# Optimization experiments

Hardware: AMD Instinct MI355X
Metric: run time of the kernel (lower is better)

Reference implementation:

```python
import jax, jax.numpy as jnp
import numpy as np

D_MODEL = 1024
NUM_HEADS = 16
HEAD_DIM = D_MODEL // NUM_HEADS
BATCH = 2
SEQ = 2048


def setup_inputs() -> dict:
    key = jax.random.key(0)
    ks = jax.random.split(key, 9)
    s = 1.0 / np.sqrt(D_MODEL)
    inp = {
        "x": jax.random.normal(ks[0], (BATCH, SEQ, D_MODEL), dtype=jnp.float32),
        "mask": jnp.ones((BATCH, SEQ), dtype=jnp.int32),
        "Wq": jax.random.uniform(ks[1], (D_MODEL, D_MODEL), jnp.float32, -s, s),
        "bq": jax.random.uniform(ks[2], (D_MODEL,), jnp.float32, -s, s),
        "Wk": jax.random.uniform(ks[3], (D_MODEL, D_MODEL), jnp.float32, -s, s),
        "bk": jax.random.uniform(ks[4], (D_MODEL,), jnp.float32, -s, s),
        "Wv": jax.random.uniform(ks[5], (D_MODEL, D_MODEL), jnp.float32, -s, s),
        "bv": jax.random.uniform(ks[6], (D_MODEL,), jnp.float32, -s, s),
        "Wo": jax.random.uniform(ks[7], (D_MODEL, D_MODEL), jnp.float32, -s, s),
        "bo": jax.random.uniform(ks[8], (D_MODEL,), jnp.float32, -s, s),
    }
    return inp


def reference(x, mask, Wq, bq, Wk, bk, Wv, bv, Wo, bo):
    B, S, D = x.shape
    H, Hd = NUM_HEADS, HEAD_DIM
    # torch Linear: y = x @ W.T + b ; then reshape to [B, H, S, Hd]
    def proj(W, b):
        return (x @ W.T + b).reshape(B, S, H, Hd).transpose(0, 2, 1, 3)
    Q = proj(Wq, bq)
    K = proj(Wk, bk)
    V = proj(Wv, bv)
    scale = 1.0 / jnp.sqrt(jnp.asarray(Hd, dtype=x.dtype))
    scores = jnp.einsum("bhqd,bhkd->bhqk", Q, K) * scale  # [B,H,S,S]
    # mask [B,S] -> broadcast over query positions; masked_fill(mask==0, -1e9)
    scores = jnp.where(mask[:, None, None, :] == 0, jnp.asarray(-1e9, x.dtype), scores)
    attn = jax.nn.softmax(scores, axis=-1)
    context = jnp.einsum("bhqk,bhkd->bhqd", attn, V)
    context = context.transpose(0, 2, 1, 3).reshape(B, S, D)
    return context @ Wo.T + bo
```

## Files before the change

### kernel.cpp

```cpp
#include <hip/hip_runtime.h>
#include <hip/hip_bf16.h>
#include <cstdint>

#define D_MODEL 1024
#define NUM_HEADS 16
#define HEAD_DIM 64
#define BATCH 2
#define SEQ 2048
#define MROWS (BATCH * SEQ)

typedef __attribute__((ext_vector_type(8))) short bf16x8;
typedef __attribute__((ext_vector_type(4))) float f32x4;
typedef __attribute__((ext_vector_type(2))) unsigned u32x2;
typedef unsigned short u16;

#define QSCALE (0.125f * 1.44269504f)

#if __has_builtin(__builtin_amdgcn_exp2f)
#define EXP2F(x) __builtin_amdgcn_exp2f(x)
#else
#define EXP2F(x) exp2f(x)
#endif

static __device__ __forceinline__ u16 f2bf(float f) {
    unsigned int u = __float_as_uint(f);
    unsigned int lsb = (u >> 16) & 1u;
    u += 0x7fffu + lsb;
    return (u16)(u >> 16);
}

#if __has_builtin(__builtin_amdgcn_cvt_pk_bf16_f32)
static __device__ __forceinline__ unsigned pkbf(float a, float b) {
    typedef __attribute__((ext_vector_type(2))) __bf16 bf2;
    union { bf2 v; unsigned u; } cv;
    cv.v = __builtin_amdgcn_cvt_pk_bf16_f32(a, b);
    return cv.u;
}
#else
static __device__ __forceinline__ unsigned pkbf(float a, float b) {
    unsigned ua = (__float_as_uint(a) + 0x8000u) >> 16;
    unsigned ub = (__float_as_uint(b) + 0x8000u) & 0xffff0000u;
    return ua | ub;
}
#endif

#if __has_builtin(__builtin_amdgcn_permlane32_swap)
static __device__ __forceinline__ void plswap32(unsigned &a, unsigned &b) {
    u32x2 r = __builtin_amdgcn_permlane32_swap(a, b, false, false);
    a = r[0]; b = r[1];
}
#else
static __device__ __forceinline__ void plswap32(unsigned &a, unsigned &b) {
    const bool lo = ((threadIdx.x & 63) < 32);
    unsigned sa = __shfl_xor((int)a, 32, 64), sb = __shfl_xor((int)b, 32, 64);
    unsigned na = lo ? a : sb;
    unsigned nb = lo ? sa : b;
    a = na; b = nb;
}
#endif
#if __has_builtin(__builtin_amdgcn_permlane16_swap)
static __device__ __forceinline__ void plswap16(unsigned &a, unsigned &b) {
    u32x2 r = __builtin_amdgcn_permlane16_swap(a, b, false, false);
    a = r[0]; b = r[1];
}
#else
static __device__ __forceinline__ void plswap16(unsigned &a, unsigned &b) {
    const bool ev = (((threadIdx.x & 63) >> 4) & 1) == 0;
    unsigned sa = __shfl_xor((int)a, 16, 64), sb = __shfl_xor((int)b, 16, 64);
    unsigned na = ev ? a : sb;
    unsigned nb = ev ? sa : b;
    a = na; b = nb;
}
#endif

static __device__ __forceinline__ void gload_lds16(const void* g, void* l) {
    __builtin_amdgcn_global_load_lds((const __attribute__((address_space(1))) unsigned int*)g,
                                     (__attribute__((address_space(3))) unsigned int*)l,
                                     16, 0, 0);
}

__global__ void cvt_all(const float* __restrict__ x,
                        const float* __restrict__ w0, const float* __restrict__ w1,
                        const float* __restrict__ w2, const float* __restrict__ w3,
                        u16* __restrict__ base) {
    const int which = blockIdx.y;
    const int NE = D_MODEL * D_MODEL;
    const float* s;
    if (which < 4)      s = x + (size_t)which * NE;
    else if (which == 4) s = w0;
    else if (which == 5) s = w1;
    else if (which == 6) s = w2;
    else                 s = w3;
    u16* dst = base + (size_t)which * NE;
    const int i = (blockIdx.x * blockDim.x + threadIdx.x) * 4;
    float4 v = *(const float4*)(s + i);
    ushort4 o;
    o.x = f2bf(v.x); o.y = f2bf(v.y); o.z = f2bf(v.z); o.w = f2bf(v.w);
    *(ushort4*)(dst + i) = o;
}

template<int BN, int MODE>
__global__ __launch_bounds__(256, 3)
void gemm_staged(const u16* __restrict__ A, const u16* __restrict__ W,
                 const float* __restrict__ b0, const float* __restrict__ b1,
                 const float* __restrict__ b2,
                 u16* __restrict__ o0, u16* __restrict__ o1, u16* __restrict__ o2,
                 float* __restrict__ of, int K, int N) {
    constexpr int WN = BN / 2;
    constexpr int NJ = WN / 16;
    __shared__ __align__(16) u16 As[128 * 64];
    __shared__ __align__(16) u16 Bs[BN * 64];
    __shared__ __align__(16) u16 T[(MODE == 0) ? 64 * 136 : 16];

    const int lane = threadIdx.x & 63;
    const int w    = threadIdx.x >> 6;
    const int quad = lane >> 4;
    const int l16  = lane & 15;
    const int wm = w >> 1, wn = w & 1;

    const u16* Ablk = A + (size_t)(blockIdx.y * 128) * K;
    const u16* Wblk = W + (size_t)(blockIdx.x * BN) * K;

    const int srow = lane >> 3;
    const int scol = lane & 7;

    f32x4 acc[4][NJ];
#pragma unroll
    for (int i = 0; i < 4; ++i)
#pragma unroll
        for (int j = 0; j < NJ; ++j) acc[i][j] = (f32x4){0.f, 0.f, 0.f, 0.f};

    for (int kb0 = 0; kb0 < K; kb0 += 64) {
        __syncthreads();
#pragma unroll
        for (int t = 0; t < 4; ++t) {
            const int r  = w * 32 + t * 8 + srow;
            const int cg = scol ^ (r & 7);
            gload_lds16(Ablk + (size_t)r * K + kb0 + cg * 8, &As[(w * 32 + t * 8) * 64]);
        }
#pragma unroll
        for (int t = 0; t < BN / 32; ++t) {
            const int r  = w * (BN / 4) + t * 8 + srow;
            const int cg = scol ^ (r & 7);
            gload_lds16(Wblk + (size_t)r * K + kb0 + cg * 8, &Bs[(w * (BN / 4) + t * 8) * 64]);
        }
        __syncthreads();
#pragma unroll
        for (int ks = 0; ks < 2; ++ks) {
            bf16x8 a[4], b[NJ];
#pragma unroll
            for (int i = 0; i < 4; ++i) {
                const int ra = wm * 64 + 16 * i + l16;
                a[i] = *(const bf16x8*)&As[ra * 64 + ((ks * 4 + quad) ^ (ra & 7)) * 8];
            }
#pragma unroll
            for (int j = 0; j < NJ; ++j) {
                const int rb = wn * WN + 16 * j + l16;
                b[j] = *(const bf16x8*)&Bs[rb * 64 + ((ks * 4 + quad) ^ (rb & 7)) * 8];
            }
#pragma unroll
            for (int i = 0; i < 4; ++i)
#pragma unroll
                for (int j = 0; j < NJ; ++j)
                    acc[i][j] = __builtin_amdgcn_mfma_f32_16x16x32_bf16(a[i], b[j], acc[i][j], 0, 0, 0);
        }
    }

    const int mbase = blockIdx.y * 128 + wm * 64;
    const int nbase = blockIdx.x * BN + wn * WN;

    if (MODE == 0 && blockIdx.x >= 16) {
        const int mb    = blockIdx.y * 128;
        const int bb    = mb >> 11;
        const int sbase = mb & 2047;
#pragma unroll
        for (int p = 0; p < 2; ++p) {
            __syncthreads();
            if (wn == p) {
#pragma unroll
                for (int j = 0; j < NJ; ++j) {
                    const int nl = 16 * j + l16;
                    const float bv = b2[(nbase + 16 * j + l16) & 1023];
#pragma unroll
                    for (int i = 0; i < 4; ++i) {
                        const int ml = wm * 64 + 16 * i + quad * 4;
                        uint2 pk;
                        pk.x = pkbf(acc[i][j][0] + bv, acc[i][j][1] + bv);
                        pk.y = pkbf(acc[i][j][2] + bv, acc[i][j][3] + bv);
                        *(uint2*)&T[nl * 136 + ml] = pk;
                    }
                }
            }
            __syncthreads();
            const int row = threadIdx.x >> 2;
            const int gn2 = blockIdx.x * 128 + p * 64 + row;
            const int rem2 = gn2 & 1023;
            const int h = rem2 >> 6, d = rem2 & 63;
            u16* dstrow = o2 + (((size_t)(bb * NUM_HEADS + h) * 64) + d) * SEQ + sbase;
#pragma unroll
            for (int k = 0; k < 4; ++k) {
                const int chunk = (threadIdx.x & 3) * 4 + k;
                *(uint4*)(dstrow + chunk * 8) = *(const uint4*)&T[row * 136 + chunk * 8];
            }
        }
        return;
    }

    if (MODE == 0) {
#pragma unroll
        for (int j = 0; j < NJ; ++j) {
            const int gn = nbase + 16 * j + l16;
            const int which = gn >> 10, rem = gn & 1023;
            const float bv = (which == 0 ? b0 : b1)[rem];
            u16* dst = (which == 0) ? o0 : o1;
            const float scl = (which == 0) ? QSCALE : 1.0f;
            const int h = rem >> 6, d = rem & 63;
#pragma unroll
            for (int i = 0; i < 4; ++i)
#pragma unroll
                for (int r = 0; r < 4; ++r) {
                    const int gm = mbase + 16 * i + quad * 4 + r;
                    const int bb = gm >> 11, s = gm & 2047;
                    dst[(((size_t)(bb * NUM_HEADS + h) * SEQ) + s) * 64 + d] =
                        f2bf((acc[i][j][r] + bv) * scl);
                }
        }
    } else {
#pragma unroll
        for (int j = 0; j < NJ; ++j) {
            const int gn = nbase + 16 * j + l16;
            const float bv = b0[gn];
#pragma unroll
            for (int i = 0; i < 4; ++i)
#pragma unroll
                for (int r = 0; r < 4; ++r) {
                    const int gm = mbase + 16 * i + quad * 4 + r;
                    of[(size_t)gm * N + gn] = acc[i][j][r] + bv;
                }
        }
    }
}

__global__ __launch_bounds__(512, 4)
void attn_kernel(const u16* __restrict__ Q, const u16* __restrict__ K,
                 const u16* __restrict__ VT, const int* __restrict__ mask,
                 u16* __restrict__ ctx) {
    __shared__ __align__(16) u16 Ks[2][64 * 64];
    __shared__ __align__(16) u16 Vs[2][64 * 64];

    const int lane = threadIdx.x & 63;
    const int w    = threadIdx.x >> 6;
    const int quad = lane >> 4;
    const int l16  = lane & 15;

    const int bh = blockIdx.x & 31;
    const int qb = blockIdx.x >> 5;
    const int b  = bh >> 4;
    const int h  = bh & 15;
    const int qbase = qb * 128 + w * 16;

    const u16* Qh = Q + (size_t)bh * SEQ * 64;
    const u16* Kh = K + (size_t)bh * SEQ * 64;
    const u16* Vh = VT + (size_t)bh * 64 * SEQ;
    const int* mrow = mask + b * SEQ;

    const int srow = lane >> 3;
    const int scol = lane & 7;
    const int cg   = scol ^ srow;

    gload_lds16(Kh + (size_t)(8 * w + srow) * 64 + cg * 8, &Ks[0][(8 * w) * 64]);
    gload_lds16(Vh + (size_t)(8 * w + srow) * SEQ + cg * 8, &Vs[0][(8 * w) * 64]);

    bf16x8 qf[2];
#pragma unroll
    for (int ks = 0; ks < 2; ++ks)
        qf[ks] = *(const bf16x8*)(Qh + (size_t)(qbase + l16) * 64 + 32 * ks + quad * 8);

    unsigned dirty = 0;
#pragma unroll
    for (int i = 0; i < 8; ++i) {
        const int4 m4 = *(const int4*)(mrow + i * 256 + lane * 4);
        const bool ok = (m4.x != 0) & (m4.y != 0) & (m4.z != 0) & (m4.w != 0);
        const unsigned long long bal = __ballot(ok);
#pragma unroll
        for (int g = 0; g < 4; ++g)
            if (((bal >> (16 * g)) & 0xffffull) != 0xffffull) dirty |= 1u << (i * 4 + g);
    }

    f32x4 o[4];
#pragma unroll
    for (int id = 0; id < 4; ++id) o[id] = (f32x4){0.f, 0.f, 0.f, 0.f};
    float lst = 0.f;
    const f32x4 fzero = (f32x4){0.f, 0.f, 0.f, 0.f};
    const int rowsel = (lane & 48) | (quad * 4);

#pragma unroll 2
    for (int kb = 0; kb < 32; ++kb) {
        const int cur = kb & 1;
        __syncthreads();

        if (kb != 31) {
            const int kn = (kb + 1) * 64;
            gload_lds16(Kh + (size_t)(kn + 8 * w + srow) * 64 + cg * 8,
                        &Ks[cur ^ 1][(8 * w) * 64]);
            gload_lds16(Vh + (size_t)(8 * w + srow) * SEQ + kn + cg * 8,
                        &Vs[cur ^ 1][(8 * w) * 64]);
        }

        const int kstart = kb * 64;
        const bool clean = ((dirty >> kb) & 1u) == 0u;

        bf16x8 kf[4][2];
#pragma unroll
        for (int ik = 0; ik < 4; ++ik) {
            const int row = 16 * ik + l16;
#pragma unroll
            for (int ks = 0; ks < 2; ++ks)
                kf[ik][ks] = *(const bf16x8*)&Ks[cur][row * 64 + ((4 * ks + quad) ^ (row & 7)) * 8];
        }

        f32x4 s[4];
        __builtin_amdgcn_s_setprio(1);
#pragma unroll
        for (int ik = 0; ik < 4; ++ik) {
            f32x4 t = __builtin_amdgcn_mfma_f32_16x16x32_bf16(kf[ik][0], qf[0], fzero, 0, 0, 0);
            t = __builtin_amdgcn_mfma_f32_16x16x32_bf16(kf[ik][1], qf[1], t, 0, 0, 0);
            s[ik] = t;
        }
        __builtin_amdgcn_s_setprio(0);

        bf16x8 vf[4][2];
#pragma unroll
        for (int id = 0; id < 4; ++id) {
            const int row = 16 * id + l16;
#pragma unroll
            for (int ks = 0; ks < 2; ++ks)
                vf[id][ks] = *(const bf16x8*)&Vs[cur][row * 64 + ((4 * ks + quad) ^ (row & 7)) * 8];
        }

        if (!clean) {
#pragma unroll
            for (int ik = 0; ik < 4; ++ik) {
                int4 mk = *(const int4*)(mrow + kstart + 16 * ik + quad * 4);
                const int* mp = (const int*)&mk;
#pragma unroll
                for (int r = 0; r < 4; ++r)
                    s[ik][r] = (mp[r] != 0) ? s[ik][r] : -1e9f;
            }
        }

        float rs = 0.f;
        unsigned c[4][2];
#pragma unroll
        for (int ik = 0; ik < 4; ++ik) {
            const float p0 = EXP2F(s[ik][0]);
            const float p1 = EXP2F(s[ik][1]);
            const float p2 = EXP2F(s[ik][2]);
            const float p3 = EXP2F(s[ik][3]);
            rs += (p0 + p1) + (p2 + p3);
            c[ik][0] = pkbf(p0, p1);
            c[ik][1] = pkbf(p2, p3);
        }
        rs += __shfl_xor(rs, 16, 64);
        rs += __shfl_xor(rs, 32, 64);
        lst += rs;

        plswap32(c[0][0], c[1][0]); plswap32(c[0][1], c[1][1]);
        plswap16(c[0][0], c[1][0]); plswap16(c[0][1], c[1][1]);
        plswap32(c[2][0], c[3][0]); plswap32(c[2][1], c[3][1]);
        plswap16(c[2][0], c[3][0]); plswap16(c[2][1], c[3][1]);
        union U { bf16x8 v; unsigned d[4]; };
        U u0, u1;
        u0.d[0] = c[0][0]; u0.d[1] = c[0][1]; u0.d[2] = c[1][0]; u0.d[3] = c[1][1];
        u1.d[0] = c[2][0]; u1.d[1] = c[2][1]; u1.d[2] = c[3][0]; u1.d[3] = c[3][1];

        __builtin_amdgcn_s_setprio(1);
#pragma unroll
        for (int ks = 0; ks < 2; ++ks) {
            const bf16x8 pf = (ks == 0) ? u0.v : u1.v;
#pragma unroll
            for (int id = 0; id < 4; ++id)
                o[id] = __builtin_amdgcn_mfma_f32_16x16x32_bf16(pf, vf[id][ks], o[id], 0, 0, 0);
        }
        __builtin_amdgcn_s_setprio(0);
    }

    float linv[4];
#pragma unroll
    for (int r = 0; r < 4; ++r) linv[r] = 1.f / __shfl(lst, rowsel + r, 64);
#pragma unroll
    for (int id = 0; id < 4; ++id)
#pragma unroll
        for (int r = 0; r < 4; ++r) {
            const int q = qbase + quad * 4 + r;
            const int d = 16 * id + l16;
            ctx[((size_t)(b * SEQ + q)) * D_MODEL + h * 64 + d] = f2bf(o[id][r] * linv[r]);
        }
}

extern "C" void kernel_launch(void* const* d_in, const int* in_sizes, int n_in,
                              void* d_out, int out_size, void* d_ws, size_t ws_size,
                              hipStream_t stream) {
    const float* x    = (const float*)d_in[0];
    const int*   mask = (const int*)d_in[1];
    const float* Wq   = (const float*)d_in[2];
    const float* bq   = (const float*)d_in[3];
    const float* Wk   = (const float*)d_in[4];
    const float* bk   = (const float*)d_in[5];
    const float* Wv   = (const float*)d_in[6];
    const float* bv   = (const float*)d_in[7];
    const float* Wo   = (const float*)d_in[8];
    const float* bo   = (const float*)d_in[9];

    u16* xb  = (u16*)d_ws;
    u16* wqb = xb  + (size_t)MROWS * D_MODEL;
    u16* wob = wqb + (size_t)3 * D_MODEL * D_MODEL;
    u16* Qb  = wob + (size_t)D_MODEL * D_MODEL;
    u16* Kb  = Qb  + (size_t)MROWS * D_MODEL;
    u16* VTb = Kb  + (size_t)MROWS * D_MODEL;
    u16* ctx = VTb + (size_t)MROWS * D_MODEL;

    cvt_all<<<dim3(D_MODEL * D_MODEL / 1024, 8), 256, 0, stream>>>(
        x, Wq, Wk, Wv, Wo, xb);

    gemm_staged<128, 0><<<dim3(3 * D_MODEL / 128, MROWS / 128), 256, 0, stream>>>(
        xb, wqb, bq, bk, bv, Qb, Kb, VTb, nullptr, D_MODEL, 3 * D_MODEL);

    attn_kernel<<<BATCH * NUM_HEADS * (SEQ / 128), 512, 0, stream>>>(Qb, Kb, VTb, mask, ctx);

    gemm_staged<64, 1><<<dim3(D_MODEL / 64, MROWS / 128), 256, 0, stream>>>(
        ctx, wob, bo, nullptr, nullptr, nullptr, nullptr, nullptr,
        (float*)d_out, D_MODEL, D_MODEL);
}
```

Baseline: 190.6 us.

## Process two query tiles per wave in attention to reuse K/V fragments

Each wave in the attention kernel now computes 32 query rows (two 16-row tiles) against every K/V block, and the block shrinks from 8 waves to 4. Each wave now stages 16 rows of K and V into shared memory. Each K and V fragment read from shared memory now feeds two MFMA streams, halving LDS reads per unit of compute. In exchange, per-wave register pressure roughly doubles for accumulators and scores, and there are fewer waves per block to hide latency.

```diff
diff --git a/kernel.cpp b/kernel.cpp
--- a/kernel.cpp
+++ b/kernel.cpp
@@ -241,7 +241,7 @@
     }
 }
 
-__global__ __launch_bounds__(512, 4)
+__global__ __launch_bounds__(256, 2)
 void attn_kernel(const u16* __restrict__ Q, const u16* __restrict__ K,
                  const u16* __restrict__ VT, const int* __restrict__ mask,
                  u16* __restrict__ ctx) {
@@ -257,7 +257,7 @@
     const int qb = blockIdx.x >> 5;
     const int b  = bh >> 4;
     const int h  = bh & 15;
-    const int qbase = qb * 128 + w * 16;
+    const int qbase = qb * 128 + w * 32;
 
     const u16* Qh = Q + (size_t)bh * SEQ * 64;
     const u16* Kh = K + (size_t)bh * SEQ * 64;
@@ -268,13 +268,22 @@
     const int scol = lane & 7;
     const int cg   = scol ^ srow;
 
-    gload_lds16(Kh + (size_t)(8 * w + srow) * 64 + cg * 8, &Ks[0][(8 * w) * 64]);
-    gload_lds16(Vh + (size_t)(8 * w + srow) * SEQ + cg * 8, &Vs[0][(8 * w) * 64]);
-
-    bf16x8 qf[2];
-#pragma unroll
-    for (int ks = 0; ks < 2; ++ks)
-        qf[ks] = *(const bf16x8*)(Qh + (size_t)(qbase + l16) * 64 + 32 * ks + quad * 8);
+    const u16* kS = Kh + (size_t)(16 * w + srow) * 64 + cg * 8;
+    const u16* vS = Vh + (size_t)(16 * w + srow) * SEQ + cg * 8;
+
+    gload_lds16(kS,            &Ks[0][(16 * w) * 64]);
+    gload_lds16(kS + 8 * 64,   &Ks[0][(16 * w + 8) * 64]);
+    gload_lds16(vS,            &Vs[0][(16 * w) * 64]);
+    gload_lds16(vS + 8 * SEQ,  &Vs[0][(16 * w + 8) * 64]);
+    kS += 64 * 64;
+    vS += 64;
+
+    bf16x8 qfA[2], qfB[2];
+#pragma unroll
+    for (int ks = 0; ks < 2; ++ks) {
+        qfA[ks] = *(const bf16x8*)(Qh + (size_t)(qbase + l16) * 64 + 32 * ks + quad * 8);
+        qfB[ks] = *(const bf16x8*)(Qh + (size_t)(qbase + 16 + l16) * 64 + 32 * ks + quad * 8);
+    }
 
     unsigned dirty = 0;
 #pragma unroll
@@ -287,12 +296,17 @@
             if (((bal >> (16 * g)) & 0xffffull) != 0xffffull) dirty |= 1u << (i * 4 + g);
     }
 
-    f32x4 o[4];
-#pragma unroll
-    for (int id = 0; id < 4; ++id) o[id] = (f32x4){0.f, 0.f, 0.f, 0.f};
-    float lst = 0.f;
+    f32x4 oA[4], oB[4];
+#pragma unroll
+    for (int id = 0; id < 4; ++id) {
+        oA[id] = (f32x4){0.f, 0.f, 0.f, 0.f};
+        oB[id] = (f32x4){0.f, 0.f, 0.f, 0.f};
+    }
+    float lstA = 0.f, lstB = 0.f;
     const f32x4 fzero = (f32x4){0.f, 0.f, 0.f, 0.f};
     const int rowsel = (lane & 48) | (quad * 4);
+
+    union U { bf16x8 v; unsigned d[4]; };
 
 #pragma unroll 2
     for (int kb = 0; kb < 32; ++kb) {
@@ -300,12 +314,13 @@
         __syncthreads();
 
         if (kb != 31) {
-            const int kn = (kb + 1) * 64;
-            gload_lds16(Kh + (size_t)(kn + 8 * w + srow) * 64 + cg * 8,
-                        &Ks[cur ^ 1][(8 * w) * 64]);
-            gload_lds16(Vh + (size_t)(8 * w + srow) * SEQ + kn + cg * 8,
-                        &Vs[cur ^ 1][(8 * w) * 64]);
-        }
+            gload_lds16(kS,           &Ks[cur ^ 1][(16 * w) * 64]);
+            gload_lds16(kS + 8 * 64,  &Ks[cur ^ 1][(16 * w + 8) * 64]);
+            gload_lds16(vS,           &Vs[cur ^ 1][(16 * w) * 64]);
+            gload_lds16(vS + 8 * SEQ, &Vs[cur ^ 1][(16 * w + 8) * 64]);
+        }
+        kS += 64 * 64;
+        vS += 64;
 
         const int kstart = kb * 64;
         const bool clean = ((dirty >> kb) & 1u) == 0u;
@@ -319,24 +334,21 @@
                 kf[ik][ks] = *(const bf16x8*)&Ks[cur][row * 64 + ((4 * ks + quad) ^ (row & 7)) * 8];
         }
 
-        f32x4 s[4];
+        f32x4 sA[4], sB[4];
         __builtin_amdgcn_s_setprio(1);
 #pragma unroll
         for (int ik = 0; ik < 4; ++ik) {
-            f32x4 t = __builtin_amdgcn_mfma_f32_16x16x32_bf16(kf[ik][0], qf[0], fzero, 0, 0, 0);
-            t = __builtin_amdgcn_mfma_f32_16x16x32_bf16(kf[ik][1], qf[1], t, 0, 0, 0);
-            s[ik] = t;
+            f32x4 t = __builtin_amdgcn_mfma_f32_16x16x32_bf16(kf[ik][0], qfA[0], fzero, 0, 0, 0);
+            t = __builtin_amdgcn_mfma_f32_16x16x32_bf16(kf[ik][1], qfA[1], t, 0, 0, 0);
+            sA[ik] = t;
+        }
+#pragma unroll
+        for (int ik = 0; ik < 4; ++ik) {
+            f32x4 t = __builtin_amdgcn_mfma_f32_16x16x32_bf16(kf[ik][0], qfB[0], fzero, 0, 0, 0);
+            t = __builtin_amdgcn_mfma_f32_16x16x32_bf16(kf[ik][1], qfB[1], t, 0, 0, 0);
+            sB[ik] = t;
         }
         __builtin_amdgcn_s_setprio(0);
-
-        bf16x8 vf[4][2];
-#pragma unroll
-        for (int id = 0; id < 4; ++id) {
-            const int row = 16 * id + l16;
-#pragma unroll
-            for (int ks = 0; ks < 2; ++ks)
-                vf[id][ks] = *(const bf16x8*)&Vs[cur][row * 64 + ((4 * ks + quad) ^ (row & 7)) * 8];
-        }
 
         if (!clean) {
 #pragma unroll
@@ -344,57 +356,84 @@
                 int4 mk = *(const int4*)(mrow + kstart + 16 * ik + quad * 4);
                 const int* mp = (const int*)&mk;
 #pragma unroll
-                for (int r = 0; r < 4; ++r)
-                    s[ik][r] = (mp[r] != 0) ? s[ik][r] : -1e9f;
-            }
-        }
-
-        float rs = 0.f;
-        unsigned c[4][2];
+                for (int r = 0; r < 4; ++r) {
+                    sA[ik][r] = (mp[r] != 0) ? sA[ik][r] : -1e9f;
+                    sB[ik][r] = (mp[r] != 0) ? sB[ik][r] : -1e9f;
+                }
+            }
+        }
+
+        float rsA = 0.f, rsB = 0.f;
+        unsigned cA[4][2], cB[4][2];
 #pragma unroll
         for (int ik = 0; ik < 4; ++ik) {
-            const float p0 = EXP2F(s[ik][0]);
-            const float p1 = EXP2F(s[ik][1]);
-            const float p2 = EXP2F(s[ik][2]);
-            const float p3 = EXP2F(s[ik][3]);
-            rs += (p0 + p1) + (p2 + p3);
-            c[ik][0] = pkbf(p0, p1);
-            c[ik][1] = pkbf(p2, p3);
-        }
-        rs += __shfl_xor(rs, 16, 64);
-        rs += __shfl_xor(rs, 32, 64);
-        lst += rs;
-
-        plswap32(c[0][0], c[1][0]); plswap32(c[0][1], c[1][1]);
-        plswap16(c[0][0], c[1][0]); plswap16(c[0][1], c[1][1]);
-        plswap32(c[2][0], c[3][0]); plswap32(c[2][1], c[3][1]);
-        plswap16(c[2][0], c[3][0]); plswap16(c[2][1], c[3][1]);
-        union U { bf16x8 v; unsigned d[4]; };
-        U u0, u1;
-        u0.d[0] = c[0][0]; u0.d[1] = c[0][1]; u0.d[2] = c[1][0]; u0.d[3] = c[1][1];
-        u1.d[0] = c[2][0]; u1.d[1] = c[2][1]; u1.d[2] = c[3][0]; u1.d[3] = c[3][1];
+            const float a0 = EXP2F(sA[ik][0]);
+            const float a1 = EXP2F(sA[ik][1]);
+            const float a2 = EXP2F(sA[ik][2]);
+            const float a3 = EXP2F(sA[ik][3]);
+            rsA += (a0 + a1) + (a2 + a3);
+            cA[ik][0] = pkbf(a0, a1);
+            cA[ik][1] = pkbf(a2, a3);
+            const float b0 = EXP2F(sB[ik][0]);
+            const float b1 = EXP2F(sB[ik][1]);
+            const float b2 = EXP2F(sB[ik][2]);
+            const float b3 = EXP2F(sB[ik][3]);
+            rsB += (b0 + b1) + (b2 + b3);
+            cB[ik][0] = pkbf(b0, b1);
+            cB[ik][1] = pkbf(b2, b3);
+        }
+        rsA += __shfl_xor(rsA, 16, 64);
+        rsA += __shfl_xor(rsA, 32, 64);
+        lstA += rsA;
+        rsB += __shfl_xor(rsB, 16, 64);
+        rsB += __shfl_xor(rsB, 32, 64);
+        lstB += rsB;
+
+        plswap32(cA[0][0], cA[1][0]); plswap32(cA[0][1], cA[1][1]);
+        plswap16(cA[0][0], cA[1][0]); plswap16(cA[0][1], cA[1][1]);
+        plswap32(cA[2][0], cA[3][0]); plswap32(cA[2][1], cA[3][1]);
+        plswap16(cA[2][0], cA[3][0]); plswap16(cA[2][1], cA[3][1]);
+        plswap32(cB[0][0], cB[1][0]); plswap32(cB[0][1], cB[1][1]);
+        plswap16(cB[0][0], cB[1][0]); plswap16(cB[0][1], cB[1][1]);
+        plswap32(cB[2][0], cB[3][0]); plswap32(cB[2][1], cB[3][1]);
+        plswap16(cB[2][0], cB[3][0]); plswap16(cB[2][1], cB[3][1]);
+        U uA0, uA1, uB0, uB1;
+        uA0.d[0] = cA[0][0]; uA0.d[1] = cA[0][1]; uA0.d[2] = cA[1][0]; uA0.d[3] = cA[1][1];
+        uA1.d[0] = cA[2][0]; uA1.d[1] = cA[2][1]; uA1.d[2] = cA[3][0]; uA1.d[3] = cA[3][1];
+        uB0.d[0] = cB[0][0]; uB0.d[1] = cB[0][1]; uB0.d[2] = cB[1][0]; uB0.d[3] = cB[1][1];
+        uB1.d[0] = cB[2][0]; uB1.d[1] = cB[2][1]; uB1.d[2] = cB[3][0]; uB1.d[3] = cB[3][1];
 
         __builtin_amdgcn_s_setprio(1);
 #pragma unroll
         for (int ks = 0; ks < 2; ++ks) {
-            const bf16x8 pf = (ks == 0) ? u0.v : u1.v;
-#pragma unroll
-            for (int id = 0; id < 4; ++id)
-                o[id] = __builtin_amdgcn_mfma_f32_16x16x32_bf16(pf, vf[id][ks], o[id], 0, 0, 0);
+            const bf16x8 pfA = (ks == 0) ? uA0.v : uA1.v;
+            const bf16x8 pfB = (ks == 0) ? uB0.v : uB1.v;
+#pragma unroll
+            for (int id = 0; id < 4; ++id) {
+                const int row = 16 * id + l16;
+                const bf16x8 vfr = *(const bf16x8*)&Vs[cur][row * 64 + ((4 * ks + quad) ^ (row & 7)) * 8];
+                oA[id] = __builtin_amdgcn_mfma_f32_16x16x32_bf16(pfA, vfr, oA[id], 0, 0, 0);
+                oB[id] = __builtin_amdgcn_mfma_f32_16x16x32_bf16(pfB, vfr, oB[id], 0, 0, 0);
+            }
         }
         __builtin_amdgcn_s_setprio(0);
     }
 
-    float linv[4];
-#pragma unroll
-    for (int r = 0; r < 4; ++r) linv[r] = 1.f / __shfl(lst, rowsel + r, 64);
+    float linvA[4], linvB[4];
+#pragma unroll
+    for (int r = 0; r < 4; ++r) {
+        linvA[r] = 1.f / __shfl(lstA, rowsel + r, 64);
+        linvB[r] = 1.f / __shfl(lstB, rowsel + r, 64);
+    }
 #pragma unroll
     for (int id = 0; id < 4; ++id)
 #pragma unroll
         for (int r = 0; r < 4; ++r) {
-            const int q = qbase + quad * 4 + r;
             const int d = 16 * id + l16;
-            ctx[((size_t)(b * SEQ + q)) * D_MODEL + h * 64 + d] = f2bf(o[id][r] * linv[r]);
+            const int qA = qbase + quad * 4 + r;
+            ctx[((size_t)(b * SEQ + qA)) * D_MODEL + h * 64 + d] = f2bf(oA[id][r] * linvA[r]);
+            const int qB = qA + 16;
+            ctx[((size_t)(b * SEQ + qB)) * D_MODEL + h * 64 + d] = f2bf(oB[id][r] * linvB[r]);
         }
 }
 
@@ -426,7 +465,7 @@
     gemm_staged<128, 0><<<dim3(3 * D_MODEL / 128, MROWS / 128), 256, 0, stream>>>(
         xb, wqb, bq, bk, bv, Qb, Kb, VTb, nullptr, D_MODEL, 3 * D_MODEL);
 
-    attn_kernel<<<BATCH * NUM_HEADS * (SEQ / 128), 512, 0, stream>>>(Qb, Kb, VTb, mask, ctx);
+    attn_kernel<<<BATCH * NUM_HEADS * (SEQ / 128), 256, 0, stream>>>(Qb, Kb, VTb, mask, ctx);
 
     gemm_staged<64, 1><<<dim3(D_MODEL / 64, MROWS / 128), 256, 0, stream>>>(
         ctx, wob, bo, nullptr, nullptr, nullptr, nullptr, nullptr,
```

After: 192.1 us. No clear change (+0.8%).

## Software-pipeline attention loop: overlap QK^T of next block with softmax-PV of previous

Applied to the files above, without the earlier changes.

Switches the K/V shared-memory ring from double to triple buffering. Each iteration now computes the QK^T scores for block kb and then runs exp/softmax and the PV MFMAs for block kb-1, with the scores carried across iterations in registers. The aim is to let the score MFMAs overlap the exp/pack VALU work and hide their latency. In exchange it uses more LDS and registers, which can lower occupancy under launch_bounds(512,4), and V fragments are now read from LDS inside the PV loop.

```diff
diff --git a/kernel.cpp b/kernel.cpp
--- a/kernel.cpp
+++ b/kernel.cpp
@@ -245,8 +245,8 @@
 void attn_kernel(const u16* __restrict__ Q, const u16* __restrict__ K,
                  const u16* __restrict__ VT, const int* __restrict__ mask,
                  u16* __restrict__ ctx) {
-    __shared__ __align__(16) u16 Ks[2][64 * 64];
-    __shared__ __align__(16) u16 Vs[2][64 * 64];
+    __shared__ __align__(16) u16 Ks[3][64 * 64];
+    __shared__ __align__(16) u16 Vs[3][64 * 64];
 
     const int lane = threadIdx.x & 63;
     const int w    = threadIdx.x >> 6;
@@ -294,72 +294,32 @@
     const f32x4 fzero = (f32x4){0.f, 0.f, 0.f, 0.f};
     const int rowsel = (lane & 48) | (quad * 4);
 
-#pragma unroll 2
-    for (int kb = 0; kb < 32; ++kb) {
-        const int cur = kb & 1;
-        __syncthreads();
-
-        if (kb != 31) {
-            const int kn = (kb + 1) * 64;
-            gload_lds16(Kh + (size_t)(kn + 8 * w + srow) * 64 + cg * 8,
-                        &Ks[cur ^ 1][(8 * w) * 64]);
-            gload_lds16(Vh + (size_t)(8 * w + srow) * SEQ + kn + cg * 8,
-                        &Vs[cur ^ 1][(8 * w) * 64]);
-        }
-
-        const int kstart = kb * 64;
-        const bool clean = ((dirty >> kb) & 1u) == 0u;
-
-        bf16x8 kf[4][2];
-#pragma unroll
-        for (int ik = 0; ik < 4; ++ik) {
-            const int row = 16 * ik + l16;
-#pragma unroll
-            for (int ks = 0; ks < 2; ++ks)
-                kf[ik][ks] = *(const bf16x8*)&Ks[cur][row * 64 + ((4 * ks + quad) ^ (row & 7)) * 8];
-        }
-
-        f32x4 s[4];
-        __builtin_amdgcn_s_setprio(1);
-#pragma unroll
-        for (int ik = 0; ik < 4; ++ik) {
-            f32x4 t = __builtin_amdgcn_mfma_f32_16x16x32_bf16(kf[ik][0], qf[0], fzero, 0, 0, 0);
-            t = __builtin_amdgcn_mfma_f32_16x16x32_bf16(kf[ik][1], qf[1], t, 0, 0, 0);
-            s[ik] = t;
-        }
-        __builtin_amdgcn_s_setprio(0);
-
-        bf16x8 vf[4][2];
-#pragma unroll
-        for (int id = 0; id < 4; ++id) {
-            const int row = 16 * id + l16;
-#pragma unroll
-            for (int ks = 0; ks < 2; ++ks)
-                vf[id][ks] = *(const bf16x8*)&Vs[cur][row * 64 + ((4 * ks + quad) ^ (row & 7)) * 8];
-        }
-
+    union U { bf16x8 v; unsigned d[4]; };
+    f32x4 sP[4];
+
+    auto softmax_pv = [&](int kbp, int p3) {
+        const bool clean = ((dirty >> kbp) & 1u) == 0u;
         if (!clean) {
 #pragma unroll
             for (int ik = 0; ik < 4; ++ik) {
-                int4 mk = *(const int4*)(mrow + kstart + 16 * ik + quad * 4);
+                int4 mk = *(const int4*)(mrow + kbp * 64 + 16 * ik + quad * 4);
                 const int* mp = (const int*)&mk;
 #pragma unroll
                 for (int r = 0; r < 4; ++r)
-                    s[ik][r] = (mp[r] != 0) ? s[ik][r] : -1e9f;
-            }
-        }
-
+                    sP[ik][r] = (mp[r] != 0) ? sP[ik][r] : -1e9f;
+            }
+        }
         float rs = 0.f;
         unsigned c[4][2];
 #pragma unroll
         for (int ik = 0; ik < 4; ++ik) {
-            const float p0 = EXP2F(s[ik][0]);
-            const float p1 = EXP2F(s[ik][1]);
-            const float p2 = EXP2F(s[ik][2]);
-            const float p3 = EXP2F(s[ik][3]);
-            rs += (p0 + p1) + (p2 + p3);
+            const float p0 = EXP2F(sP[ik][0]);
+            const float p1 = EXP2F(sP[ik][1]);
+            const float p2 = EXP2F(sP[ik][2]);
+            const float p3v = EXP2F(sP[ik][3]);
+            rs += (p0 + p1) + (p2 + p3v);
             c[ik][0] = pkbf(p0, p1);
-            c[ik][1] = pkbf(p2, p3);
+            c[ik][1] = pkbf(p2, p3v);
         }
         rs += __shfl_xor(rs, 16, 64);
         rs += __shfl_xor(rs, 32, 64);
@@ -369,7 +329,6 @@
         plswap16(c[0][0], c[1][0]); plswap16(c[0][1], c[1][1]);
         plswap32(c[2][0], c[3][0]); plswap32(c[2][1], c[3][1]);
         plswap16(c[2][0], c[3][0]); plswap16(c[2][1], c[3][1]);
-        union U { bf16x8 v; unsigned d[4]; };
         U u0, u1;
         u0.d[0] = c[0][0]; u0.d[1] = c[0][1]; u0.d[2] = c[1][0]; u0.d[3] = c[1][1];
         u1.d[0] = c[2][0]; u1.d[1] = c[2][1]; u1.d[2] = c[3][0]; u1.d[3] = c[3][1];
@@ -379,11 +338,54 @@
         for (int ks = 0; ks < 2; ++ks) {
             const bf16x8 pf = (ks == 0) ? u0.v : u1.v;
 #pragma unroll
-            for (int id = 0; id < 4; ++id)
-                o[id] = __builtin_amdgcn_mfma_f32_16x16x32_bf16(pf, vf[id][ks], o[id], 0, 0, 0);
+            for (int id = 0; id < 4; ++id) {
+                const int row = 16 * id + l16;
+                const bf16x8 vfr = *(const bf16x8*)&Vs[p3][row * 64 + ((4 * ks + quad) ^ (row & 7)) * 8];
+                o[id] = __builtin_amdgcn_mfma_f32_16x16x32_bf16(pf, vfr, o[id], 0, 0, 0);
+            }
         }
         __builtin_amdgcn_s_setprio(0);
+    };
+
+#pragma unroll 3
+    for (int kb = 0; kb < 32; ++kb) {
+        const int cur = kb % 3;
+        __syncthreads();
+
+        if (kb != 31) {
+            const int nxt = (kb + 1) % 3;
+            const int kn = (kb + 1) * 64;
+            gload_lds16(Kh + (size_t)(kn + 8 * w + srow) * 64 + cg * 8,
+                        &Ks[nxt][(8 * w) * 64]);
+            gload_lds16(Vh + (size_t)(8 * w + srow) * SEQ + kn + cg * 8,
+                        &Vs[nxt][(8 * w) * 64]);
+        }
+
+        bf16x8 kf[4][2];
+#pragma unroll
+        for (int ik = 0; ik < 4; ++ik) {
+            const int row = 16 * ik + l16;
+#pragma unroll
+            for (int ks = 0; ks < 2; ++ks)
+                kf[ik][ks] = *(const bf16x8*)&Ks[cur][row * 64 + ((4 * ks + quad) ^ (row & 7)) * 8];
+        }
+
+        f32x4 sN[4];
+        __builtin_amdgcn_s_setprio(1);
+#pragma unroll
+        for (int ik = 0; ik < 4; ++ik) {
+            f32x4 t = __builtin_amdgcn_mfma_f32_16x16x32_bf16(kf[ik][0], qf[0], fzero, 0, 0, 0);
+            t = __builtin_amdgcn_mfma_f32_16x16x32_bf16(kf[ik][1], qf[1], t, 0, 0, 0);
+            sN[ik] = t;
+        }
+        __builtin_amdgcn_s_setprio(0);
+
+        if (kb > 0) softmax_pv(kb - 1, (kb - 1) % 3);
+
+#pragma unroll
+        for (int ik = 0; ik < 4; ++ik) sP[ik] = sN[ik];
     }
+    softmax_pv(31, 31 % 3);
 
     float linv[4];
 #pragma unroll
```

Measured after the change: 196.2 us. 1.03x slower.
